# Kernel optimization log

Hardware: AMD Instinct MI355X
Metric: run time of the kernel (lower is better)

## Reference

```python
import jax, jax.numpy as jnp
import numpy as np

NP_, NT_, NA_, NG_ = 50000, 200000, 20000, 500
ED, HID, H, C, L = 64, 64, 4, 16, 2
NEG_SLOPE = 0.2


def _edges(key, e, ns, nd):
    k1, k2 = jax.random.split(key)
    return jnp.stack([jax.random.randint(k1, (e,), 0, ns, dtype=jnp.int32),
                      jax.random.randint(k2, (e,), 0, nd, dtype=jnp.int32)])


def setup_inputs() -> dict:
    key = jax.random.key(0)
    ks = iter(jax.random.split(key, 64))
    nrm = lambda shp, s=0.1: (jax.random.normal(next(ks), shp, jnp.float32) * s)
    inp = {
        'playlist_x': nrm((NP_, 8), 1.0), 'track_x': nrm((NT_, 7), 1.0),
        'artist_x': nrm((NA_, 1), 1.0), 'genre_x': nrm((NG_, NG_), 1.0),
        'emb_playlist': nrm((NP_, ED)), 'emb_artist': nrm((NA_, ED)),
        'pf_W': nrm((8, ED)), 'pf_b': jnp.zeros((ED,)),
        'tf_W': nrm((7, ED)), 'tf_b': jnp.zeros((ED,)),
        'af_W': nrm((1, ED)), 'af_b': jnp.zeros((ED,)),
        'gf_W': nrm((NG_, ED)), 'gf_b': jnp.zeros((ED,)),
        'ip_W_playlist': nrm((2 * ED, HID)), 'ip_b_playlist': jnp.zeros((HID,)),
        'ip_W_track': nrm((ED, HID)), 'ip_b_track': jnp.zeros((HID,)),
        'ip_W_artist': nrm((2 * ED, HID)), 'ip_b_artist': jnp.zeros((HID,)),
        'ip_W_genre': nrm((ED, HID)), 'ip_b_genre': jnp.zeros((HID,)),
        # 8 relations x L layers, shared lin per relation (PyG GATConv with int in_channels)
        'gat_W': nrm((L, 8, HID, H * C)), 'gat_b': jnp.zeros((L, 8, H * C)),
        'gat_as': nrm((L, 8, H, C)), 'gat_ad': nrm((L, 8, H, C)),
        'ln_w': jnp.ones((L, HID)), 'ln_b': jnp.zeros((L, HID)),
        'op_W_playlist': nrm((HID, ED)), 'op_b_playlist': jnp.zeros((ED,)),
        'op_W_track': nrm((HID, ED)), 'op_b_track': jnp.zeros((ED,)),
        'op_W_artist': nrm((HID, ED)), 'op_b_artist': jnp.zeros((ED,)),
        'op_W_genre': nrm((HID, ED)), 'op_b_genre': jnp.zeros((ED,)),
        'playlist_idx': jnp.arange(NP_, dtype=jnp.int32),
        'artist_idx': jnp.arange(NA_, dtype=jnp.int32),
        'ei_contains': _edges(next(ks), 1000000, NP_, NT_),
        'ei_in_playlist': _edges(next(ks), 1000000, NT_, NP_),
        'ei_by': _edges(next(ks), 200000, NT_, NA_),
        'ei_created': _edges(next(ks), 200000, NA_, NT_),
        'ei_has_genre': _edges(next(ks), 600000, NT_, NG_),
        'ei_includes': _edges(next(ks), 600000, NG_, NT_),
        'ei_performs': _edges(next(ks), 60000, NA_, NG_),
        'ei_performed_by': _edges(next(ks), 60000, NG_, NA_),
    }
    return inp


def _gat(x_src, x_dst, ei, W, b, a_s, a_d, n_dst):
    # PyG GATConv: shared lin, edge softmax over dst, scatter-add aggregation
    hs = (x_src @ W).reshape(x_src.shape[0], H, C)
    hd = (x_dst @ W).reshape(x_dst.shape[0], H, C)
    es, ed = ei[0], ei[1]
    al_s = jnp.einsum('nhc,hc->nh', hs, a_s)  # [Ns,H]
    al_d = jnp.einsum('nhc,hc->nh', hd, a_d)  # [Nd,H]
    alpha = jax.nn.leaky_relu(al_s[es] + al_d[ed], NEG_SLOPE)  # [E,H]
    amax = jax.ops.segment_max(alpha, ed, num_segments=n_dst)
    amax = jnp.where(jnp.isfinite(amax), amax, 0.0)
    ex = jnp.exp(alpha - amax[ed])
    den = jax.ops.segment_sum(ex, ed, num_segments=n_dst)
    coef = ex / (den[ed] + 1e-16)
    msg = (hs[es] * coef[:, :, None]).reshape(es.shape[0], H * C)  # [E,H*C]
    return jax.ops.segment_sum(msg, ed, num_segments=n_dst) + b


def _ln(x, w, b):
    m = jnp.mean(x, -1, keepdims=True)
    v = jnp.mean((x - m) ** 2, -1, keepdims=True)
    return (x - m) * jax.lax.rsqrt(v + 1e-5) * w + b


def _forward(playlist_x, track_x, artist_x, genre_x, emb_playlist, emb_artist,
             pf_W, pf_b, tf_W, tf_b, af_W, af_b, gf_W, gf_b,
             ip_W_playlist, ip_b_playlist, ip_W_track, ip_b_track,
             ip_W_artist, ip_b_artist, ip_W_genre, ip_b_genre,
             gat_W, gat_b, gat_as, gat_ad, ln_w, ln_b,
             op_W_playlist, op_b_playlist, op_W_track, op_b_track,
             op_W_artist, op_b_artist, op_W_genre, op_b_genre,
             playlist_idx, artist_idx, ei_contains, ei_in_playlist, ei_by,
             ei_created, ei_has_genre, ei_includes, ei_performs, ei_performed_by):
    h_p = jnp.concatenate([emb_playlist[playlist_idx], playlist_x @ pf_W + pf_b], -1) @ ip_W_playlist + ip_b_playlist
    h_t = (track_x @ tf_W + tf_b) @ ip_W_track + ip_b_track
    h_a = jnp.concatenate([emb_artist[artist_idx], artist_x @ af_W + af_b], -1) @ ip_W_artist + ip_b_artist
    h_g = (genre_x @ gf_W + gf_b) @ ip_W_genre + ip_b_genre
    for i in range(L):
        pp, pt, pa, pg = h_p, h_t, h_a, h_g
        g = lambda r, xs, xd, ei, nd: _gat(xs, xd, ei, gat_W[i, r], gat_b[i, r], gat_as[i, r], gat_ad[i, r], nd)
        # relation index: 0 contains,1 in_playlist,2 by,3 created,4 has_genre,5 includes_track,6 performs_genre,7 performed_by
        nt = g(0, pp, pt, ei_contains, NT_) + g(3, pa, pt, ei_created, NT_) + g(5, pg, pt, ei_includes, NT_)
        np2 = g(1, pt, pp, ei_in_playlist, NP_)
        na = g(2, pt, pa, ei_by, NA_) + g(7, pg, pa, ei_performed_by, NA_)
        ng = g(4, pt, pg, ei_has_genre, NG_) + g(6, pa, pg, ei_performs, NG_)
        h_p, h_t, h_a, h_g = jax.nn.relu(np2), jax.nn.relu(nt), jax.nn.relu(na), jax.nn.relu(ng)
        if i > 0:  # residual only after first layer (matches `if i > 0`)
            h_p, h_t, h_a, h_g = h_p + pp, h_t + pt, h_a + pa, h_g + pg
        h_p, h_t, h_a, h_g = (_ln(v, ln_w[i], ln_b[i]) for v in (h_p, h_t, h_a, h_g))
    return jnp.concatenate([
        h_p @ op_W_playlist + op_b_playlist,
        h_t @ op_W_track + op_b_track,
        h_a @ op_W_artist + op_b_artist,
        h_g @ op_W_genre + op_b_genre], axis=0)  # [NP+NT+NA+NG, 64]


def reference(playlist_x, track_x, artist_x, genre_x, emb_playlist, emb_artist,
              pf_W, pf_b, tf_W, tf_b, af_W, af_b, gf_W, gf_b,
              ip_W_playlist, ip_b_playlist, ip_W_track, ip_b_track,
              ip_W_artist, ip_b_artist, ip_W_genre, ip_b_genre,
              gat_W, gat_b, gat_as, gat_ad, ln_w, ln_b,
              op_W_playlist, op_b_playlist, op_W_track, op_b_track,
              op_W_artist, op_b_artist, op_W_genre, op_b_genre,
              playlist_idx, artist_idx, ei_contains, ei_in_playlist, ei_by,
              ei_created, ei_has_genre, ei_includes, ei_performs, ei_performed_by):
    return _forward(playlist_x, track_x, artist_x, genre_x, emb_playlist, emb_artist,
                    pf_W, pf_b, tf_W, tf_b, af_W, af_b, gf_W, gf_b,
                    ip_W_playlist, ip_b_playlist, ip_W_track, ip_b_track,
                    ip_W_artist, ip_b_artist, ip_W_genre, ip_b_genre,
                    gat_W, gat_b, gat_as, gat_ad, ln_w, ln_b,
                    op_W_playlist, op_b_playlist, op_W_track, op_b_track,
                    op_W_artist, op_b_artist, op_W_genre, op_b_genre,
                    playlist_idx, artist_idx, ei_contains, ei_in_playlist, ei_by,
                    ei_created, ei_has_genre, ei_includes, ei_performs, ei_performed_by)
```

## Files before the change

kernel.cpp:

```cpp
#include <hip/hip_runtime.h>
#include <cstdint>

constexpr int NP=50000, NT=200000, NA=20000, NG=500;
constexpr int NTOT = NP+NT+NA+NG;
constexpr int RO_P=0, RO_T=NP, RO_A=NP+NT, RO_G=NP+NT+NA;
constexpr int E_TOT = 3720000;

constexpr int H_E [8] = {1000000,1000000,200000,200000,600000,600000,60000,60000};
constexpr int H_ES[9] = {0,1000000,2000000,2200000,2400000,3000000,3600000,3660000,3720000};
constexpr int H_NS[8] = {NP,NT,NT,NA,NT,NG,NA,NG};
constexpr int H_ND[8] = {NT,NP,NA,NT,NG,NT,NG,NA};
constexpr int H_SO[8] = {RO_P,RO_T,RO_T,RO_A,RO_T,RO_G,RO_A,RO_G};
constexpr int H_DO[8] = {RO_T,RO_P,RO_A,RO_T,RO_G,RO_T,RO_G,RO_A};
constexpr int H_RPO[8]= {0,200001,250002,270003,470004,470505,670506,671007};
constexpr int H_CO[8] = {0,200000,250000,270000,470000,470500,670500,671000};

__constant__ int c_E [8] = {1000000,1000000,200000,200000,600000,600000,60000,60000};
__constant__ int c_ES[9] = {0,1000000,2000000,2200000,2400000,3000000,3600000,3660000,3720000};
__constant__ int c_ND[8] = {200000,50000,20000,200000,500,200000,500,20000};
__constant__ int c_RPO[8]= {0,200001,250002,270003,470004,470505,670506,671007};
__constant__ int c_CO[8] = {0,200000,250000,270000,470000,470500,670500,671000};

__constant__ int sb_pref[9] = {0,196,245,265,461,462,658,659,679};
constexpr int SB_BLOCKS = 679;

constexpr int WSZ = 16384;
__constant__ int c_G [8] = {16,16,4,4,10,10,2,2};
__constant__ int c_CS[8] = {62500,62500,50000,50000,60000,60000,30000,30000};
__constant__ int c_NW[8] = {13,4,2,13,1,13,1,2};
__constant__ int gw_pref[9] = {0,208,272,280,332,342,472,474,478};
constexpr int GW_BLOCKS = 478;
__constant__ int c_C2[8] = {0,3200000,4000000,4080000,4880000,4885000,6885000,6886000};

constexpr int OWT=0;
constexpr int OBT=448;
constexpr int OWPX=512;
constexpr int OBP=1024;
constexpr int OAV=1088;
constexpr int OBA=1152;
constexpr int OBG=1216;
constexpr int OBAGG=1280;
constexpr int OWAS=1792;
constexpr int OWAD=5888;
constexpr int OWG=9984;

struct EiPtrs { const int* p[8]; };

__device__ __forceinline__ unsigned short f2bf(float f){
  unsigned u = __float_as_uint(f);
  u += 0x7FFF + ((u>>16)&1);
  return (unsigned short)(u>>16);
}
__device__ __forceinline__ float bf2f(unsigned short b){
  return __uint_as_float(((unsigned)b)<<16);
}

__global__ __launch_bounds__(256) void k_prep(
  const float* __restrict__ pf_W, const float* __restrict__ pf_b,
  const float* __restrict__ tf_W, const float* __restrict__ tf_b,
  const float* __restrict__ af_W, const float* __restrict__ af_b,
  const float* __restrict__ gf_W, const float* __restrict__ gf_b,
  const float* __restrict__ ipWp, const float* __restrict__ ipbp,
  const float* __restrict__ ipWt, const float* __restrict__ ipbt,
  const float* __restrict__ ipWa, const float* __restrict__ ipba,
  const float* __restrict__ ipWg, const float* __restrict__ ipbg,
  const float* __restrict__ gatW, const float* __restrict__ gatB,
  const float* __restrict__ gatAs, const float* __restrict__ gatAd,
  float* __restrict__ cb)
{
  int tid = blockIdx.x*256 + threadIdx.x;
  int STR = gridDim.x*256;
  for(int i=tid;i<7*64;i+=STR){ int j=i>>6,c=i&63; float s=0.f;
    for(int k=0;k<64;k++) s += tf_W[j*64+k]*ipWt[k*64+c];
    cb[OWT+i]=s; }
  for(int i=tid;i<64;i+=STR){ float s=ipbt[i];
    for(int k=0;k<64;k++) s += tf_b[k]*ipWt[k*64+i];
    cb[OBT+i]=s; }
  for(int i=tid;i<8*64;i+=STR){ int j=i>>6,c=i&63; float s=0.f;
    for(int k=0;k<64;k++) s += pf_W[j*64+k]*ipWp[(64+k)*64+c];
    cb[OWPX+i]=s; }
  for(int i=tid;i<64;i+=STR){ float s=ipbp[i];
    for(int k=0;k<64;k++) s += pf_b[k]*ipWp[(64+k)*64+i];
    cb[OBP+i]=s; }
  for(int i=tid;i<64;i+=STR){ float s=0.f;
    for(int k=0;k<64;k++) s += af_W[k]*ipWa[(64+k)*64+i];
    cb[OAV+i]=s; }
  for(int i=tid;i<64;i+=STR){ float s=ipba[i];
    for(int k=0;k<64;k++) s += af_b[k]*ipWa[(64+k)*64+i];
    cb[OBA+i]=s; }
  for(int i=tid;i<64;i+=STR){ float s=ipbg[i];
    for(int k=0;k<64;k++) s += gf_b[k]*ipWg[k*64+i];
    cb[OBG+i]=s; }
  for(int i=tid;i<512;i+=STR){ int l=i>>8, t=(i>>6)&3, c=i&63;
    const float* B = gatB + l*8*64; float s;
    if(t==0)      s = B[1*64+c];
    else if(t==1) s = B[0*64+c]+B[3*64+c]+B[5*64+c];
    else if(t==2) s = B[2*64+c]+B[7*64+c];
    else          s = B[4*64+c]+B[6*64+c];
    cb[OBAGG+i]=s; }
  for(int i=tid;i<2*8*64*4;i+=STR){ int h=i&3, k=(i>>2)&63, lr=i>>8;
    const float* as = gatAs + lr*64;
    cb[OWAS+i] = ((k>>4)==h) ? as[h*16 + (k&15)] : 0.f;
    const float* W  = gatW + (size_t)lr*4096;
    const float* ad = gatAd + lr*64 + h*16;
    float d=0.f;
    for(int c=0;c<16;c++){ d += W[k*64+h*16+c]*ad[c]; }
    cb[OWAD+i]=d; }
  for(int i=tid;i<512*64;i+=STR){ int g=i>>6,c=i&63; float s=0.f;
    if(g<500){ for(int k=0;k<64;k++) s += gf_W[g*64+k]*ipWg[k*64+c]; }
    cb[OWG+i]=s; }
}

#define MM_DECL  __shared__ float sX[64*65]; __shared__ float sW[64*68]; \
  int tid=threadIdx.x; int rt=(tid>>4)<<2, ct=(tid&15)<<2; float acc[4][4];

#define MM_LOOP() \
  _Pragma("unroll 8") \
  for(int k=0;k<64;k++){ \
    float4 wv = *(const float4*)&sW[k*68+ct]; \
    float x0=sX[(rt+0)*65+k], x1=sX[(rt+1)*65+k], x2=sX[(rt+2)*65+k], x3=sX[(rt+3)*65+k]; \
    acc[0][0]+=x0*wv.x; acc[0][1]+=x0*wv.y; acc[0][2]+=x0*wv.z; acc[0][3]+=x0*wv.w; \
    acc[1][0]+=x1*wv.x; acc[1][1]+=x1*wv.y; acc[1][2]+=x1*wv.z; acc[1][3]+=x1*wv.w; \
    acc[2][0]+=x2*wv.x; acc[2][1]+=x2*wv.y; acc[2][2]+=x2*wv.z; acc[2][3]+=x2*wv.w; \
    acc[3][0]+=x3*wv.x; acc[3][1]+=x3*wv.y; acc[3][2]+=x3*wv.z; acc[3][3]+=x3*wv.w; \
  }

template<bool ALS, bool B16>
__global__ __launch_bounds__(256) void k_mm64(const float* __restrict__ X, const float* __restrict__ W,
  const float* __restrict__ bias, float* __restrict__ Y, float* __restrict__ alsY,
  const float* __restrict__ was, int N)
{
  MM_DECL
  int row0 = blockIdx.x*64;
  for(int i=tid;i<4096;i+=256){
    int r=i>>6, k=i&63;
    sX[r*65+k] = (row0+r<N)? X[(size_t)(row0+r)*64+k] : 0.f;
    sW[r*68+k] = W[i];
  }
  __syncthreads();
  #pragma unroll
  for(int i=0;i<4;i++){ acc[i][0]=0.f;acc[i][1]=0.f;acc[i][2]=0.f;acc[i][3]=0.f; }
  MM_LOOP()
  float4 bv = make_float4(0.f,0.f,0.f,0.f);
  if(bias) bv = *(const float4*)&bias[ct];
  #pragma unroll
  for(int i=0;i<4;i++){
    int row=row0+rt+i;
    if(row<N){
      if(B16){
        ushort4 o;
        o.x=f2bf(acc[i][0]+bv.x); o.y=f2bf(acc[i][1]+bv.y);
        o.z=f2bf(acc[i][2]+bv.z); o.w=f2bf(acc[i][3]+bv.w);
        *(ushort4*)&((unsigned short*)Y)[(size_t)row*64+ct] = o;
      } else {
        *(float4*)&Y[(size_t)row*64+ct] =
          make_float4(acc[i][0]+bv.x, acc[i][1]+bv.y, acc[i][2]+bv.z, acc[i][3]+bv.w);
      }
    }
  }
  if(ALS){
    float4 w0 = *(const float4*)&was[(ct+0)*4];
    float4 w1 = *(const float4*)&was[(ct+1)*4];
    float4 w2 = *(const float4*)&was[(ct+2)*4];
    float4 w3 = *(const float4*)&was[(ct+3)*4];
    #pragma unroll
    for(int i=0;i<4;i++){
      float4 p;
      p.x = acc[i][0]*w0.x + acc[i][1]*w1.x + acc[i][2]*w2.x + acc[i][3]*w3.x;
      p.y = acc[i][0]*w0.y + acc[i][1]*w1.y + acc[i][2]*w2.y + acc[i][3]*w3.y;
      p.z = acc[i][0]*w0.z + acc[i][1]*w1.z + acc[i][2]*w2.z + acc[i][3]*w3.z;
      p.w = acc[i][0]*w0.w + acc[i][1]*w1.w + acc[i][2]*w2.w + acc[i][3]*w3.w;
      #pragma unroll
      for(int m=1;m<16;m<<=1){
        p.x+=__shfl_xor(p.x,m); p.y+=__shfl_xor(p.y,m);
        p.z+=__shfl_xor(p.z,m); p.w+=__shfl_xor(p.w,m);
      }
      int row=row0+rt+i;
      if((tid&15)==0 && row<N) *(float4*)&alsY[(size_t)row*4] = p;
    }
  }
}

constexpr int BP=(NP+63)/64, BT=(NT+63)/64, BA=(NA+63)/64;
__global__ __launch_bounds__(256) void k_init(
  const float* __restrict__ px, const float* __restrict__ tx, const float* __restrict__ ax,
  const float* __restrict__ embp, const float* __restrict__ emba,
  const int* __restrict__ pidx, const int* __restrict__ aidx,
  const float* __restrict__ ipWp, const float* __restrict__ ipWa,
  const float* __restrict__ cb, float* __restrict__ hout)
{
  MM_DECL
  __shared__ float sE[64*9];
  int bid = blockIdx.x;
  if(bid < BP){
    int row0 = bid*64;
    for(int i=tid;i<4096;i+=256){
      int r=i>>6,k=i&63; int row=row0+r;
      sX[r*65+k] = (row<NP)? embp[(size_t)pidx[row]*64+k] : 0.f;
      sW[r*68+k] = ipWp[i];
    }
    for(int i=tid;i<512;i+=256){ int r=i>>3,j=i&7; int row=row0+r;
      sE[r*9+j] = (row<NP)? px[(size_t)row*8+j] : 0.f; }
    __syncthreads();
    { float4 b = *(const float4*)&cb[OBP+ct];
      #pragma unroll
      for(int i=0;i<4;i++){ acc[i][0]=b.x;acc[i][1]=b.y;acc[i][2]=b.z;acc[i][3]=b.w; } }
    #pragma unroll
    for(int j=0;j<8;j++){
      float4 w = *(const float4*)&cb[OWPX + j*64 + ct];
      #pragma unroll
      for(int i=0;i<4;i++){ float xe = sE[(rt+i)*9+j];
        acc[i][0]+=xe*w.x; acc[i][1]+=xe*w.y; acc[i][2]+=xe*w.z; acc[i][3]+=xe*w.w; }
    }
    MM_LOOP()
    #pragma unroll
    for(int i=0;i<4;i++){ int row=row0+rt+i;
      if(row<NP) *(float4*)&hout[(size_t)(RO_P+row)*64+ct] =
        make_float4(acc[i][0],acc[i][1],acc[i][2],acc[i][3]); }
  } else if(bid < BP+BT){
    int row0 = (bid-BP)*64;
    for(int i=tid;i<512;i+=256){ int r=i>>3,j=i&7; int row=row0+r;
      sE[r*9+j] = (row<NT && j<7)? tx[(size_t)row*7+j] : 0.f; }
    __syncthreads();
    { float4 b = *(const float4*)&cb[OBT+ct];
      #pragma unroll
      for(int i=0;i<4;i++){ acc[i][0]=b.x;acc[i][1]=b.y;acc[i][2]=b.z;acc[i][3]=b.w; } }
    #pragma unroll
    for(int j=0;j<7;j++){
      float4 w = *(const float4*)&cb[OWT + j*64 + ct];
      #pragma unroll
      for(int i=0;i<4;i++){ float xe = sE[(rt+i)*9+j];
        acc[i][0]+=xe*w.x; acc[i][1]+=xe*w.y; acc[i][2]+=xe*w.z; acc[i][3]+=xe*w.w; }
    }
    #pragma unroll
    for(int i=0;i<4;i++){ int row=row0+rt+i;
      if(row<NT) *(float4*)&hout[(size_t)(RO_T+row)*64+ct] =
        make_float4(acc[i][0],acc[i][1],acc[i][2],acc[i][3]); }
  } else {
    int row0 = (bid-BP-BT)*64;
    for(int i=tid;i<4096;i+=256){
      int r=i>>6,k=i&63; int row=row0+r;
      sX[r*65+k] = (row<NA)? emba[(size_t)aidx[row]*64+k] : 0.f;
      sW[r*68+k] = ipWa[i];
    }
    for(int i=tid;i<64;i+=256){ int row=row0+i; sE[i] = (row<NA)? ax[row] : 0.f; }
    __syncthreads();
    #pragma unroll
    for(int i=0;i<4;i++){
      float4 b = *(const float4*)&cb[OBA+ct];
      float4 av = *(const float4*)&cb[OAV+ct];
      float xe = sE[rt+i];
      acc[i][0]=b.x+xe*av.x; acc[i][1]=b.y+xe*av.y; acc[i][2]=b.z+xe*av.z; acc[i][3]=b.w+xe*av.w;
    }
    MM_LOOP()
    #pragma unroll
    for(int i=0;i<4;i++){ int row=row0+rt+i;
      if(row<NA) *(float4*)&hout[(size_t)(RO_A+row)*64+ct] =
        make_float4(acc[i][0],acc[i][1],acc[i][2],acc[i][3]); }
  }
}

__global__ __launch_bounds__(256) void k_init_g(const float* __restrict__ gx,
  const float* __restrict__ cb, float* __restrict__ hout)
{
  int wid = (blockIdx.x<<2)|(threadIdx.x>>6);
  int lane = threadIdx.x&63;
  if(wid>=NG) return;
  float acc = cb[OBG+lane];
  const float* WG = cb+OWG;
  for(int kb=0;kb<512;kb+=64){
    int k = kb+lane;
    float xv = (k<500)? gx[(size_t)wid*500+k] : 0.f;
    for(int j=0;j<64;j++){
      float x = __shfl(xv, j);
      acc += x * WG[(size_t)(kb+j)*64+lane];
    }
  }
  hout[(size_t)(RO_G+wid)*64+lane] = acc;
}

__global__ __launch_bounds__(1024) void k_cnt2(EiPtrs ei, int* __restrict__ cnt2){
  __shared__ int wcnt[WSZ];
  int bid=blockIdx.x, tid=threadIdx.x;
  int r=0;
  #pragma unroll
  for(int q=1;q<8;q++) if(bid>=gw_pref[q]) r=q;
  int local = bid - gw_pref[r];
  int NW=c_NW[r];
  int g = local/NW, w = local-g*NW;
  int lo=w*WSZ, nd=c_ND[r], n=min(WSZ,nd-lo);
  for(int i=tid;i<n;i+=1024) wcnt[i]=0;
  __syncthreads();
  int E=c_E[r], CS=c_CS[r];
  int e0=g*CS, e1=min(e0+CS,E);
  const int* __restrict__ pd = ei.p[r]+E;
  for(int e=e0+tid;e<e1;e+=1024){
    int d = pd[e]-lo;
    if((unsigned)d < (unsigned)n) atomicAdd(&wcnt[d],1);
  }
  __syncthreads();
  int* c = cnt2 + c_C2[r] + g*nd + lo;
  for(int i=tid;i<n;i+=1024) c[i]=wcnt[i];
}

__global__ __launch_bounds__(1024) void k_scan1(const int* __restrict__ cnt2, int* __restrict__ bsum){
  int bid = blockIdx.x;
  int r=0;
  #pragma unroll
  for(int q=1;q<8;q++) if(bid>=sb_pref[q]) r=q;
  int lb = bid - sb_pref[r];
  int nd = c_ND[r];
  int idx = lb*1024 + threadIdx.x;
  int v = 0;
  if(idx<nd){
    int G=c_G[r]; int base=c_C2[r]+idx;
    for(int g=0;g<G;g++) v += cnt2[base+g*nd];
  }
  #pragma unroll
  for(int m=1;m<64;m<<=1) v += __shfl_xor(v,m);
  __shared__ int wsum[16];
  int lane = threadIdx.x&63, wid=threadIdx.x>>6;
  if(lane==0) wsum[wid]=v;
  __syncthreads();
  if(threadIdx.x==0){
    int s=0;
    #pragma unroll
    for(int w=0;w<16;w++) s+=wsum[w];
    bsum[bid]=s;
  }
}

__global__ __launch_bounds__(256) void k_scan2(int* __restrict__ bsum, int* __restrict__ rowptr){
  int r = blockIdx.x;
  int nb = sb_pref[r+1]-sb_pref[r];
  __shared__ int s[200];
  int tid=threadIdx.x;
  if(tid<nb) s[tid]=bsum[sb_pref[r]+tid];
  __syncthreads();
  if(tid==0){
    int run=0;
    for(int i=0;i<nb;i++){ int t=s[i]; s[i]=run; run+=t; }
    rowptr[c_RPO[r]+c_ND[r]] = run;
  }
  __syncthreads();
  if(tid<nb) bsum[sb_pref[r]+tid]=s[tid];
}

__global__ __launch_bounds__(1024) void k_scan3(const int* __restrict__ cnt2, const int* __restrict__ bsum,
  int* __restrict__ rowptr){
  int bid = blockIdx.x;
  int r=0;
  #pragma unroll
  for(int q=1;q<8;q++) if(bid>=sb_pref[q]) r=q;
  int lb = bid - sb_pref[r];
  int nd = c_ND[r];
  int tid = threadIdx.x;
  int idx = lb*1024 + tid;
  int v = 0;
  if(idx<nd){
    int G=c_G[r]; int base=c_C2[r]+idx;
    for(int g=0;g<G;g++) v += cnt2[base+g*nd];
  }
  __shared__ int s[1024];
  s[tid]=v;
  __syncthreads();
  #pragma unroll
  for(int off=1;off<1024;off<<=1){
    int t = (tid>=off)? s[tid-off] : 0;
    __syncthreads();
    s[tid]+=t;
    __syncthreads();
  }
  int ex = s[tid]-v + bsum[bid];
  if(idx<nd) rowptr[c_RPO[r]+idx]=ex;
}

__global__ __launch_bounds__(1024) void k_off2(const int* __restrict__ rowptr, int* __restrict__ cnt2){
  int bid = blockIdx.x;
  int r=0;
  #pragma unroll
  for(int q=1;q<8;q++) if(bid>=sb_pref[q]) r=q;
  int idx = (bid-sb_pref[r])*1024 + threadIdx.x;
  int nd = c_ND[r];
  if(idx<nd){
    int run = rowptr[c_RPO[r]+idx];
    int G=c_G[r]; int base=c_C2[r]+idx;
    for(int g=0;g<G;g++){
      int t = cnt2[base+g*nd];
      cnt2[base+g*nd] = run;
      run += t;
    }
  }
}

__global__ __launch_bounds__(1024) void k_scat2(EiPtrs ei, const int* __restrict__ off2,
  int* __restrict__ col){
  __shared__ int wcur[WSZ];
  int bid=blockIdx.x, tid=threadIdx.x;
  int r=0;
  #pragma unroll
  for(int q=1;q<8;q++) if(bid>=gw_pref[q]) r=q;
  int local = bid - gw_pref[r];
  int NW=c_NW[r];
  int g = local/NW, w = local-g*NW;
  int lo=w*WSZ, nd=c_ND[r], n=min(WSZ,nd-lo);
  const int* o = off2 + c_C2[r] + g*nd + lo;
  for(int i=tid;i<n;i+=1024) wcur[i]=o[i];
  __syncthreads();
  int E=c_E[r], CS=c_CS[r];
  int e0=g*CS, e1=min(e0+CS,E);
  const int* __restrict__ ps = ei.p[r];
  const int* __restrict__ pd = ps+E;
  int* cl = col + c_ES[r];
  for(int e=e0+tid;e<e1;e+=1024){
    int d = pd[e]-lo;
    if((unsigned)d < (unsigned)n){
      int pos = atomicAdd(&wcur[d],1);
      cl[pos] = ps[e];
    }
  }
}

template<bool FIRST, bool LAST>
__global__ __launch_bounds__(256) void k_agg(const int* __restrict__ rp, const int* __restrict__ col,
  const unsigned short* __restrict__ hs, const float* __restrict__ als,
  const float* __restrict__ Xd, const float* __restrict__ wad,
  float* __restrict__ out, int nd,
  const float* __restrict__ bagg, const float* __restrict__ lnw,
  const float* __restrict__ lnb, int resid)
{
  int wid = (blockIdx.x<<2)|(threadIdx.x>>6);
  int lane = threadIdx.x&63;
  if(wid>=nd) return;
  float x = Xd[(size_t)wid*64+lane];
  float4 wv = *(const float4*)&wad[lane*4];
  float a0=x*wv.x, a1=x*wv.y, a2=x*wv.z, a3=x*wv.w;
  #pragma unroll
  for(int m=1;m<64;m<<=1){
    a0+=__shfl_xor(a0,m); a1+=__shfl_xor(a1,m); a2+=__shfl_xor(a2,m); a3+=__shfl_xor(a3,m);
  }
  int h = lane>>4;
  float adv = (h==0)?a0:(h==1)?a1:(h==2)?a2:a3;
  int start = rp[wid], end = rp[wid+1];
  float den=0.f, acc=0.f;
  int j = start;
  for(; j+4<=end; j+=4){
    int s0=col[j], s1=col[j+1], s2=col[j+2], s3=col[j+3];
    float A0=als[(size_t)s0*4+h], A1=als[(size_t)s1*4+h];
    float A2=als[(size_t)s2*4+h], A3=als[(size_t)s3*4+h];
    float h0=bf2f(hs[(size_t)s0*64+lane]), h1=bf2f(hs[(size_t)s1*64+lane]);
    float h2=bf2f(hs[(size_t)s2*64+lane]), h3=bf2f(hs[(size_t)s3*64+lane]);
    float v0=A0+adv; v0=fmaxf(v0,0.2f*v0); float e0=__expf(v0);
    float v1=A1+adv; v1=fmaxf(v1,0.2f*v1); float e1=__expf(v1);
    float v2=A2+adv; v2=fmaxf(v2,0.2f*v2); float e2=__expf(v2);
    float v3=A3+adv; v3=fmaxf(v3,0.2f*v3); float e3=__expf(v3);
    den+=e0; acc+=e0*h0;
    den+=e1; acc+=e1*h1;
    den+=e2; acc+=e2*h2;
    den+=e3; acc+=e3*h3;
  }
  for(; j<end; j++){
    int s = col[j];
    float ah = als[(size_t)s*4+h] + adv;
    ah = fmaxf(ah, 0.2f*ah);
    float e = __expf(ah);
    den += e;
    acc += e*bf2f(hs[(size_t)s*64+lane]);
  }
  float r = acc/(den+1e-16f);
  size_t idx = (size_t)wid*64+lane;
  if(!LAST){
    if(FIRST) out[idx] = r;
    else      out[idx] += r;
  } else {
    float v = FIRST ? r : (out[idx] + r);
    v += bagg[lane];
    v = fmaxf(v, 0.f);
    if(resid) v += x;
    float s = v;
    #pragma unroll
    for(int m=1;m<64;m<<=1) s += __shfl_xor(s,m);
    float mu = s*(1.f/64.f);
    float d = v-mu;
    float q = d*d;
    #pragma unroll
    for(int m=1;m<64;m<<=1) q += __shfl_xor(q,m);
    float var = q*(1.f/64.f);
    out[idx] = d*rsqrtf(var+1e-5f)*lnw[lane] + lnb[lane];
  }
}

template<bool FIRST, bool LAST>
__global__ __launch_bounds__(1024) void k_agg_blk(const int* __restrict__ rp, const int* __restrict__ col,
  const unsigned short* __restrict__ hs, const float* __restrict__ als,
  const float* __restrict__ Xd, const float* __restrict__ wad,
  float* __restrict__ out, int nd,
  const float* __restrict__ bagg, const float* __restrict__ lnw,
  const float* __restrict__ lnb, int resid)
{
  int d = blockIdx.x;
  if(d>=nd) return;
  int tid=threadIdx.x, lane=tid&63, wid=tid>>6;
  __shared__ float sden[16*4];
  __shared__ float sacc[16][64];
  float x = Xd[(size_t)d*64+lane];
  float4 wv = *(const float4*)&wad[lane*4];
  float a0=x*wv.x, a1=x*wv.y, a2=x*wv.z, a3=x*wv.w;
  #pragma unroll
  for(int m=1;m<64;m<<=1){
    a0+=__shfl_xor(a0,m); a1+=__shfl_xor(a1,m); a2+=__shfl_xor(a2,m); a3+=__shfl_xor(a3,m);
  }
  int h = lane>>4;
  float adv = (h==0)?a0:(h==1)?a1:(h==2)?a2:a3;
  int start = rp[d], end = rp[d+1];
  float den=0.f, acc=0.f;
  int j = start+wid;
  for(; j+48<end; j+=64){
    int s0=col[j], s1=col[j+16], s2=col[j+32], s3=col[j+48];
    float A0=als[(size_t)s0*4+h], A1=als[(size_t)s1*4+h];
    float A2=als[(size_t)s2*4+h], A3=als[(size_t)s3*4+h];
    float h0=bf2f(hs[(size_t)s0*64+lane]), h1=bf2f(hs[(size_t)s1*64+lane]);
    float h2=bf2f(hs[(size_t)s2*64+lane]), h3=bf2f(hs[(size_t)s3*64+lane]);
    float v0=A0+adv; v0=fmaxf(v0,0.2f*v0); float e0=__expf(v0);
    float v1=A1+adv; v1=fmaxf(v1,0.2f*v1); float e1=__expf(v1);
    float v2=A2+adv; v2=fmaxf(v2,0.2f*v2); float e2=__expf(v2);
    float v3=A3+adv; v3=fmaxf(v3,0.2f*v3); float e3=__expf(v3);
    den+=e0; acc+=e0*h0;
    den+=e1; acc+=e1*h1;
    den+=e2; acc+=e2*h2;
    den+=e3; acc+=e3*h3;
  }
  for(; j<end; j+=16){
    int s = col[j];
    float ah = als[(size_t)s*4+h] + adv;
    ah = fmaxf(ah, 0.2f*ah);
    float e = __expf(ah);
    den += e;
    acc += e*bf2f(hs[(size_t)s*64+lane]);
  }
  if((lane&15)==0) sden[wid*4+h]=den;
  sacc[wid][lane]=acc;
  __syncthreads();
  if(tid<64){
    float s=0.f, dt=0.f;
    #pragma unroll
    for(int w=0;w<16;w++){ s+=sacc[w][tid]; dt+=sden[w*4+(tid>>4)]; }
    float r = s/(dt+1e-16f);
    size_t idx = (size_t)d*64+tid;
    if(!LAST){
      if(FIRST) out[idx] = r;
      else      out[idx] += r;
    } else {
      float v = FIRST ? r : (out[idx] + r);
      v += bagg[tid];
      v = fmaxf(v, 0.f);
      if(resid) v += x;
      float sv = v;
      #pragma unroll
      for(int m=1;m<64;m<<=1) sv += __shfl_xor(sv,m);
      float mu = sv*(1.f/64.f);
      float dd = v-mu;
      float q = dd*dd;
      #pragma unroll
      for(int m=1;m<64;m<<=1) q += __shfl_xor(q,m);
      float var = q*(1.f/64.f);
      out[idx] = dd*rsqrtf(var+1e-5f)*lnw[tid] + lnb[tid];
    }
  }
}

extern "C" void kernel_launch(void* const* d_in, const int* in_sizes, int n_in,
                              void* d_out, int out_size, void* d_ws, size_t ws_size,
                              hipStream_t stream)
{
  const float* playlist_x=(const float*)d_in[0];
  const float* track_x   =(const float*)d_in[1];
  const float* artist_x  =(const float*)d_in[2];
  const float* genre_x   =(const float*)d_in[3];
  const float* embp=(const float*)d_in[4];
  const float* emba=(const float*)d_in[5];
  const float* pf_W=(const float*)d_in[6];  const float* pf_b=(const float*)d_in[7];
  const float* tf_W=(const float*)d_in[8];  const float* tf_b=(const float*)d_in[9];
  const float* af_W=(const float*)d_in[10]; const float* af_b=(const float*)d_in[11];
  const float* gf_W=(const float*)d_in[12]; const float* gf_b=(const float*)d_in[13];
  const float* ipWp=(const float*)d_in[14]; const float* ipbp=(const float*)d_in[15];
  const float* ipWt=(const float*)d_in[16]; const float* ipbt=(const float*)d_in[17];
  const float* ipWa=(const float*)d_in[18]; const float* ipba=(const float*)d_in[19];
  const float* ipWg=(const float*)d_in[20]; const float* ipbg=(const float*)d_in[21];
  const float* gatW=(const float*)d_in[22]; const float* gatB=(const float*)d_in[23];
  const float* gatAs=(const float*)d_in[24];const float* gatAd=(const float*)d_in[25];
  const float* lnw=(const float*)d_in[26];  const float* lnb=(const float*)d_in[27];
  const float* opWp=(const float*)d_in[28]; const float* opbp=(const float*)d_in[29];
  const float* opWt=(const float*)d_in[30]; const float* opbt=(const float*)d_in[31];
  const float* opWa=(const float*)d_in[32]; const float* opba=(const float*)d_in[33];
  const float* opWg=(const float*)d_in[34]; const float* opbg=(const float*)d_in[35];
  const int* pidx=(const int*)d_in[36];
  const int* aidx=(const int*)d_in[37];
  EiPtrs ei;
  for(int r=0;r<8;r++) ei.p[r]=(const int*)d_in[38+r];

  char* ws=(char*)d_ws;
  float* hA=(float*)d_out;
  float* cb = (float*)ws;

  size_t o_hB  = 256*1024;
  size_t o_hs  = o_hB + (size_t)NTOT*64*4;
  unsigned short* hs16 = (unsigned short*)(ws+o_hs);
  size_t o_als = o_hs + (size_t)NT*64*2;
  float* als=(float*)(ws+o_als);
  size_t o_rp  = o_als + (size_t)NT*4*4;
  int* rowptr=(int*)(ws+o_rp);
  size_t o_col = o_rp + 691008*4;
  int* col=(int*)(ws+o_col);
  int* cnt2=(int*)(ws+o_hs);
  int* bsum=cnt2+6926000;
  float* hB = (float*)(ws+o_hB);

  k_prep<<<128,256,0,stream>>>(pf_W,pf_b,tf_W,tf_b,af_W,af_b,gf_W,gf_b,
      ipWp,ipbp,ipWt,ipbt,ipWa,ipba,ipWg,ipbg,gatW,gatB,gatAs,gatAd,cb);
  k_init<<<BP+BT+BA,256,0,stream>>>(playlist_x,track_x,artist_x,embp,emba,pidx,aidx,ipWp,ipWa,cb,hA);
  k_init_g<<<(NG+3)/4,256,0,stream>>>(genre_x,cb,hA);

  k_cnt2<<<GW_BLOCKS,1024,0,stream>>>(ei,cnt2);
  k_scan1<<<SB_BLOCKS,1024,0,stream>>>(cnt2,bsum);
  k_scan2<<<8,256,0,stream>>>(bsum,rowptr);
  k_scan3<<<SB_BLOCKS,1024,0,stream>>>(cnt2,bsum,rowptr);
  k_off2<<<SB_BLOCKS,1024,0,stream>>>(rowptr,cnt2);
  k_scat2<<<GW_BLOCKS,1024,0,stream>>>(ei,cnt2,col);

  for(int l=0;l<2;l++){
    float* hcur = l? hB : hA;
    float* hnew = l? hA : hB;
    const float* lw = lnw + l*64;
    const float* lb = lnb + l*64;
    for(int r=0;r<8;r++){
      int Ns=H_NS[r], Nd=H_ND[r];
      const float* Xs = hcur + (size_t)H_SO[r]*64;
      const float* Xd = hcur + (size_t)H_DO[r]*64;
      const float* W  = gatW + (size_t)(l*8+r)*4096;
      const float* was = cb+OWAS+(size_t)(l*8+r)*256;
      const float* wad = cb+OWAD+(size_t)(l*8+r)*256;
      float* outp = hnew + (size_t)H_DO[r]*64;
      int t = (r==1)?0 : (r==0||r==3||r==5)?1 : (r==2||r==7)?2 : 3;
      const float* bagg = cb + OBAGG + l*256 + t*64;
      k_mm64<true,true><<<(Ns+63)/64,256,0,stream>>>(Xs,W,nullptr,(float*)hs16,als,was,Ns);
      if(r==4){
        k_agg_blk<true ,false><<<Nd,1024,0,stream>>>(rowptr+H_RPO[r], col+H_ES[r], hs16, als, Xd, wad, outp, Nd, bagg, lw, lb, l);
      } else if(r==6){
        k_agg_blk<false,true ><<<Nd,1024,0,stream>>>(rowptr+H_RPO[r], col+H_ES[r], hs16, als, Xd, wad, outp, Nd, bagg, lw, lb, l);
      } else if(r==0 || r==2){
        k_agg<true ,false><<<(Nd+3)/4,256,0,stream>>>(rowptr+H_RPO[r], col+H_ES[r], hs16, als, Xd, wad, outp, Nd, bagg, lw, lb, l);
      } else if(r==3){
        k_agg<false,false><<<(Nd+3)/4,256,0,stream>>>(rowptr+H_RPO[r], col+H_ES[r], hs16, als, Xd, wad, outp, Nd, bagg, lw, lb, l);
      } else if(r==1){
        k_agg<true ,true ><<<(Nd+3)/4,256,0,stream>>>(rowptr+H_RPO[r], col+H_ES[r], hs16, als, Xd, wad, outp, Nd, bagg, lw, lb, l);
      } else {
        k_agg<false,true ><<<(Nd+3)/4,256,0,stream>>>(rowptr+H_RPO[r], col+H_ES[r], hs16, als, Xd, wad, outp, Nd, bagg, lw, lb, l);
      }
    }
  }
  k_mm64<false,false><<<(NP+63)/64,256,0,stream>>>(hA+(size_t)RO_P*64, opWp, opbp, hA+(size_t)RO_P*64, nullptr, nullptr, NP);
  k_mm64<false,false><<<(NT+63)/64,256,0,stream>>>(hA+(size_t)RO_T*64, opWt, opbt, hA+(size_t)RO_T*64, nullptr, nullptr, NT);
  k_mm64<false,false><<<(NA+63)/64,256,0,stream>>>(hA+(size_t)RO_A*64, opWa, opba, hA+(size_t)RO_A*64, nullptr, nullptr, NA);
  k_mm64<false,false><<<(NG+63)/64,256,0,stream>>>(hA+(size_t)RO_G*64, opWg, opbg, hA+(size_t)RO_G*64, nullptr, nullptr, NG);
}
```

Measured before the change: 1.369 ms.

## Pre-partition edges by destination window before CSR count and scatter

Adds a coarse partitioning pass that buckets each relation's edges by 16K-destination window. It uses per-chunk counts, a serial offset scan and a partition kernel that writes source ids and 16-bit local destinations. The windowed count and scatter kernels then read only their own bucket instead of scanning the whole edge chunk once per window, which removes the redundant reads of up to 13 windows. In exchange it adds three kernels, including a single-thread scan, plus extra workspace traffic for the partitioned arrays. The partition order is nondeterministic because it comes from atomics, which may change the col order within a row.

```diff
diff --git a/kernel.cpp b/kernel.cpp
--- a/kernel.cpp
+++ b/kernel.cpp
@@ -29,7 +29,9 @@
 __constant__ int c_CS[8] = {62500,62500,50000,50000,60000,60000,30000,30000};
 __constant__ int c_NW[8] = {13,4,2,13,1,13,1,2};
 __constant__ int gw_pref[9] = {0,208,272,280,332,342,472,474,478};
+__constant__ int ch_pref[9] = {0,16,32,36,40,50,60,62,64};
 constexpr int GW_BLOCKS = 478;
+constexpr int CH_BLOCKS = 64;
 __constant__ int c_C2[8] = {0,3200000,4000000,4080000,4880000,4885000,6885000,6886000};
 
 constexpr int OWT=0;
@@ -279,7 +281,66 @@
   hout[(size_t)(RO_G+wid)*64+lane] = acc;
 }
 
-__global__ __launch_bounds__(1024) void k_cnt2(EiPtrs ei, int* __restrict__ cnt2){
+__global__ __launch_bounds__(1024) void k_bcnt(EiPtrs ei, int* __restrict__ bcnt){
+  __shared__ int pcnt[16][16];
+  int bid=blockIdx.x, tid=threadIdx.x;
+  int r=0;
+  #pragma unroll
+  for(int q=1;q<8;q++) if(bid>=ch_pref[q]) r=q;
+  int g = bid - ch_pref[r];
+  if(tid<256) ((int*)pcnt)[tid]=0;
+  __syncthreads();
+  int wave = tid>>6;
+  int E=c_E[r], CS=c_CS[r];
+  int e0=g*CS, e1=min(e0+CS,E);
+  const int* __restrict__ pd = ei.p[r]+E;
+  for(int e=e0+tid;e<e1;e+=1024){
+    int w = pd[e]>>14;
+    atomicAdd(&pcnt[wave][w],1);
+  }
+  __syncthreads();
+  if(tid<16 && tid<c_NW[r]){
+    int s=0;
+    #pragma unroll
+    for(int wv=0;wv<16;wv++) s+=pcnt[wv][tid];
+    bcnt[gw_pref[r] + g*c_NW[r] + tid] = s;
+  }
+}
+
+__global__ void k_bscan(const int* __restrict__ bcnt, int* __restrict__ bofs){
+  if(threadIdx.x==0 && blockIdx.x==0){
+    int run=0;
+    for(int i=0;i<GW_BLOCKS;i++){ bofs[i]=run; run+=bcnt[i]; }
+    bofs[GW_BLOCKS]=run;
+  }
+}
+
+__global__ __launch_bounds__(1024) void k_part(EiPtrs ei, const int* __restrict__ bofs,
+  int* __restrict__ esrc, unsigned short* __restrict__ edl){
+  __shared__ int pofs[16];
+  int bid=blockIdx.x, tid=threadIdx.x;
+  int r=0;
+  #pragma unroll
+  for(int q=1;q<8;q++) if(bid>=ch_pref[q]) r=q;
+  int g = bid - ch_pref[r];
+  int NW=c_NW[r];
+  if(tid<NW) pofs[tid] = bofs[gw_pref[r] + g*NW + tid];
+  __syncthreads();
+  int E=c_E[r], CS=c_CS[r];
+  int e0=g*CS, e1=min(e0+CS,E);
+  const int* __restrict__ ps = ei.p[r];
+  const int* __restrict__ pd = ps+E;
+  for(int e=e0+tid;e<e1;e+=1024){
+    int dst = pd[e];
+    int w = dst>>14;
+    int pos = atomicAdd(&pofs[w],1);
+    esrc[pos] = ps[e];
+    edl[pos] = (unsigned short)(dst & 16383);
+  }
+}
+
+__global__ __launch_bounds__(1024) void k_cntw(const int* __restrict__ bofs,
+  const unsigned short* __restrict__ edl, int* __restrict__ cnt2){
   __shared__ int wcnt[WSZ];
   int bid=blockIdx.x, tid=threadIdx.x;
   int r=0;
@@ -291,13 +352,8 @@
   int lo=w*WSZ, nd=c_ND[r], n=min(WSZ,nd-lo);
   for(int i=tid;i<n;i+=1024) wcnt[i]=0;
   __syncthreads();
-  int E=c_E[r], CS=c_CS[r];
-  int e0=g*CS, e1=min(e0+CS,E);
-  const int* __restrict__ pd = ei.p[r]+E;
-  for(int e=e0+tid;e<e1;e+=1024){
-    int d = pd[e]-lo;
-    if((unsigned)d < (unsigned)n) atomicAdd(&wcnt[d],1);
-  }
+  int s0=bofs[bid], s1=bofs[bid+1];
+  for(int j=s0+tid;j<s1;j+=1024) atomicAdd(&wcnt[edl[j]],1);
   __syncthreads();
   int* c = cnt2 + c_C2[r] + g*nd + lo;
   for(int i=tid;i<n;i+=1024) c[i]=wcnt[i];
@@ -393,8 +449,9 @@
   }
 }
 
-__global__ __launch_bounds__(1024) void k_scat2(EiPtrs ei, const int* __restrict__ off2,
-  int* __restrict__ col){
+__global__ __launch_bounds__(1024) void k_scatw(const int* __restrict__ bofs,
+  const int* __restrict__ esrc, const unsigned short* __restrict__ edl,
+  const int* __restrict__ off2, int* __restrict__ col){
   __shared__ int wcur[WSZ];
   int bid=blockIdx.x, tid=threadIdx.x;
   int r=0;
@@ -407,17 +464,11 @@
   const int* o = off2 + c_C2[r] + g*nd + lo;
   for(int i=tid;i<n;i+=1024) wcur[i]=o[i];
   __syncthreads();
-  int E=c_E[r], CS=c_CS[r];
-  int e0=g*CS, e1=min(e0+CS,E);
-  const int* __restrict__ ps = ei.p[r];
-  const int* __restrict__ pd = ps+E;
+  int s0=bofs[bid], s1=bofs[bid+1];
   int* cl = col + c_ES[r];
-  for(int e=e0+tid;e<e1;e+=1024){
-    int d = pd[e]-lo;
-    if((unsigned)d < (unsigned)n){
-      int pos = atomicAdd(&wcur[d],1);
-      cl[pos] = ps[e];
-    }
+  for(int j=s0+tid;j<s1;j+=1024){
+    int pos = atomicAdd(&wcur[edl[j]],1);
+    cl[pos] = esrc[j];
   }
 }
 
@@ -612,6 +663,13 @@
   int* rowptr=(int*)(ws+o_rp);
   size_t o_col = o_rp + 691008*4;
   int* col=(int*)(ws+o_col);
+  size_t o_esrc= o_col + (size_t)E_TOT*4;
+  int* esrc=(int*)(ws+o_esrc);
+  size_t o_edl = o_esrc + (size_t)E_TOT*4;
+  unsigned short* edl=(unsigned short*)(ws+o_edl);
+  size_t o_bc  = o_edl + (size_t)E_TOT*2;
+  int* bcnt=(int*)(ws+o_bc);
+  int* bofs=bcnt+GW_BLOCKS;
   int* cnt2=(int*)(ws+o_hs);
   int* bsum=cnt2+6926000;
   float* hB = (float*)(ws+o_hB);
@@ -621,12 +679,15 @@
   k_init<<<BP+BT+BA,256,0,stream>>>(playlist_x,track_x,artist_x,embp,emba,pidx,aidx,ipWp,ipWa,cb,hA);
   k_init_g<<<(NG+3)/4,256,0,stream>>>(genre_x,cb,hA);
 
-  k_cnt2<<<GW_BLOCKS,1024,0,stream>>>(ei,cnt2);
+  k_bcnt<<<CH_BLOCKS,1024,0,stream>>>(ei,bcnt);
+  k_bscan<<<1,64,0,stream>>>(bcnt,bofs);
+  k_part<<<CH_BLOCKS,1024,0,stream>>>(ei,bofs,esrc,edl);
+  k_cntw<<<GW_BLOCKS,1024,0,stream>>>(bofs,edl,cnt2);
   k_scan1<<<SB_BLOCKS,1024,0,stream>>>(cnt2,bsum);
   k_scan2<<<8,256,0,stream>>>(bsum,rowptr);
   k_scan3<<<SB_BLOCKS,1024,0,stream>>>(cnt2,bsum,rowptr);
   k_off2<<<SB_BLOCKS,1024,0,stream>>>(rowptr,cnt2);
-  k_scat2<<<GW_BLOCKS,1024,0,stream>>>(ei,cnt2,col);
+  k_scatw<<<GW_BLOCKS,1024,0,stream>>>(bofs,esrc,edl,cnt2,col);
 
   for(int l=0;l<2;l++){
     float* hcur = l? hB : hA;
```

Result: slower. 1.494 ms (+9.1%).
